# Optimization experiments

Hardware: AMD Instinct MI355X
Metric: run time of the kernel (lower is better)

Reference implementation:

```python
import jax, jax.numpy as jnp
import numpy as np

B, C, L, V, H, HEADS, ITERS = 8, 2048, 3, 512, 256, 8, 8
HD = H // HEADS
MAX_LIT = 1024  # literal embedding table holds 2*MAX_LIT rows


def _lin(x, W, b):
    return x @ W.T + b


def _gelu(x):
    return jax.nn.gelu(x, approximate=False)  # torch nn.GELU default = exact erf


def _ln(x, g, b):
    m = x.mean(-1, keepdims=True)
    v = ((x - m) ** 2).mean(-1, keepdims=True)
    return (x - m) / jnp.sqrt(v + 1e-5) * g + b


def setup_inputs() -> dict:
    key = jax.random.key(0)
    ks = jax.random.split(key, 16)
    s = 0.02
    p = {}
    p["formula"] = jax.random.randint(ks[0], (B, C, L), 0, 2 * V)
    p["lit_emb"] = jax.random.normal(ks[1], (2 * MAX_LIT, H)) * s
    # clause_encoder: Linear(H,2H) -> LayerNorm(2H) -> GELU -> Linear(2H,H)
    p["ce_w1"] = jax.random.normal(ks[2], (2 * H, H)) * s
    p["ce_b1"] = jnp.zeros((2 * H,))
    p["ce_g"] = jnp.ones((2 * H,))
    p["ce_beta"] = jnp.zeros((2 * H,))
    p["ce_w2"] = jax.random.normal(ks[3], (H, 2 * H)) * s
    p["ce_b2"] = jnp.zeros((H,))
    # clause_var_attention (nn.MultiheadAttention, eval mode -> no dropout)
    p["attn_in_w"] = jax.random.normal(ks[4], (3 * H, H)) * s
    p["attn_in_b"] = jnp.zeros((3 * H,))
    p["attn_out_w"] = jax.random.normal(ks[5], (H, H)) * s
    p["attn_out_b"] = jnp.zeros((H,))
    # variable_selector: Linear -> GELU -> Linear(H,1)
    p["vs_w1"] = jax.random.normal(ks[6], (H, H)) * s
    p["vs_b1"] = jnp.zeros((H,))
    p["vs_w2"] = jax.random.normal(ks[7], (1, H)) * s
    p["vs_b2"] = jnp.zeros((1,))
    # assignment_predictor: Linear -> GELU -> Linear(H,2) -> Softmax
    p["ap_w1"] = jax.random.normal(ks[8], (H, H)) * s
    p["ap_b1"] = jnp.zeros((H,))
    p["ap_w2"] = jax.random.normal(ks[9], (2, H)) * s
    p["ap_b2"] = jnp.zeros((2,))
    # sat_predictor: Linear -> GELU -> Linear(H,1) -> Sigmoid
    p["sp_w1"] = jax.random.normal(ks[10], (H, H)) * s
    p["sp_b1"] = jnp.zeros((H,))
    p["sp_w2"] = jax.random.normal(ks[11], (1, H)) * s
    p["sp_b2"] = jnp.zeros((1,))
    return p


def _mha(q, kv, in_w, in_b, out_w, out_b):
    Wq, Wk, Wv = jnp.split(in_w, 3, axis=0)
    bq, bk, bv = jnp.split(in_b, 3, axis=0)
    Bq, Nq, _ = q.shape
    Nk = kv.shape[1]
    qh = _lin(q, Wq, bq).reshape(Bq, Nq, HEADS, HD).transpose(0, 2, 1, 3)
    kh = _lin(kv, Wk, bk).reshape(Bq, Nk, HEADS, HD).transpose(0, 2, 1, 3)
    vh = _lin(kv, Wv, bv).reshape(Bq, Nk, HEADS, HD).transpose(0, 2, 1, 3)
    attn = jax.nn.softmax(jnp.einsum("bhqd,bhkd->bhqk", qh, kh) / np.float32(np.sqrt(HD)), axis=-1)
    o = jnp.einsum("bhqk,bhkd->bhqd", attn, vh).transpose(0, 2, 1, 3).reshape(Bq, Nq, H)
    return _lin(o, out_w, out_b)


def reference(formula, lit_emb, ce_w1, ce_b1, ce_g, ce_beta, ce_w2, ce_b2,
              attn_in_w, attn_in_b, attn_out_w, attn_out_b,
              vs_w1, vs_b1, vs_w2, vs_b2, ap_w1, ap_b1, ap_w2, ap_b2,
              sp_w1, sp_b1, sp_w2, sp_b2):
    bidx = jnp.arange(B)
    lit_e = lit_emb[formula]  # [B,C,L,H]
    # clause_encoder output is assignment-independent -> hoist out of the loop
    base = _lin(_gelu(_ln(_lin(lit_e.mean(2), ce_w1, ce_b1), ce_g, ce_beta)), ce_w2, ce_b2)  # [B,C,H]
    var_idx = formula // 2  # [B,C,L]
    pol = formula % 2

    def step(carry, _):
        assignments, var_states, done = carry
        va = assignments[bidx[:, None, None], var_idx]          # [B,C,L] gather
        sat = jnp.any((va == pol) & (va != 2), -1)              # [B,C]
        clause_states = base * (1.0 - 0.9 * sat[..., None].astype(base.dtype))
        vs = _mha(var_states, clause_states, attn_in_w, attn_in_b, attn_out_w, attn_out_b)  # [B,V,H]
        scores = _lin(_gelu(_lin(vs, vs_w1, vs_b1)), vs_w2, vs_b2)[..., 0]  # [B,V]
        scores = scores + (assignments != 2).astype(scores.dtype) * (-1e9)
        sel = jnp.argmax(scores, 1)                             # [B]
        sel_states = vs[bidx, sel]
        probs = jax.nn.softmax(_lin(_gelu(_lin(sel_states, ap_w1, ap_b1)), ap_w2, ap_b2), -1)
        new_a = jnp.argmax(probs, 1).astype(assignments.dtype)
        a2 = assignments.at[bidx, sel].set(new_a)
        # conflict check with updated assignments
        va2 = a2[bidx[:, None, None], var_idx]
        sat2 = jnp.any((va2 == pol) & (va2 != 2), -1)
        conflicting = jnp.all(va2 != 2, -1) & ~sat2             # [B,C]
        any_conf = jnp.any(conflicting)                         # global, as in torch list check
        a3 = jnp.where(any_conf, a2.at[bidx, sel].set(2), a2)   # unassign selected var on conflict
        finished = jnp.all(a3 != 2) & ~any_conf                 # torch early-break condition
        assignments_n = jnp.where(done, assignments, a3)        # freeze after break
        vs_n = jnp.where(done, var_states, vs)
        return (assignments_n, vs_n, done | finished), None

    init = (jnp.full((B, V), 2, jnp.int32), jnp.zeros((B, V, H), base.dtype), jnp.array(False))
    (assignments, var_states, _), _ = jax.lax.scan(step, init, None, length=ITERS)
    is_sat = jax.nn.sigmoid(_lin(_gelu(_lin(var_states.mean(1), sp_w1, sp_b1)), sp_w2, sp_b2))  # [B,1]
    return is_sat, assignments
```

## Files before the change

kernel.cpp:

```cpp
#include <hip/hip_runtime.h>
#include <hip/hip_bf16.h>

#pragma clang fp contract(off)

#define DEVI __device__ __forceinline__

constexpr int Bc = 8, Cc = 2048, Vc = 512, Hc = 256;

constexpr int W_N = 23;
constexpr int W_OFF[W_N] = {
  0,        524288,  655360,  655872,  656384,  656896,  787968,  788224,
  984832,   985600,  1051136, 1051392, 1116928, 1117184, 1117440, 1117444,
  1182980,  1183236, 1183748, 1183752, 1249288, 1249544, 1249800 };
constexpr int W_SZ[W_N] = {
  524288, 131072, 512, 512, 512, 131072, 256, 196608, 768,
  65536, 256, 65536, 256, 256, 1, 65536, 256, 512, 2, 65536, 256, 256, 1 };
constexpr int W_TOT = 1249804;

constexpr size_t WT1_O   = 1249808;
constexpr size_t WT2_O   = WT1_O   + 131072;
constexpr size_t WTIN_O  = WT2_O   + 131072;
constexpr size_t WTOUT_O = WTIN_O  + 196608;
constexpr size_t WTV1_O  = WTOUT_O + 65536;
constexpr size_t WTAP_O  = WTV1_O  + 65536;
constexpr size_t WTSP_O  = WTAP_O  + 65536;
constexpr size_t WCK_O   = WTSP_O  + 65536;
constexpr size_t WCV_O   = WCK_O   + 131072;
constexpr size_t BCK_O   = WCV_O   + 131072;
constexpr size_t BCV_O   = BCK_O   + 256;
constexpr size_t LP_O    = BCV_O   + 256;
constexpr size_t KB_O    = LP_O    + 524288;
constexpr size_t VB_O    = KB_O    + 4194304;
constexpr size_t VS8_O   = VB_O    + 4194304;
constexpr size_t OP_O    = VS8_O   + 2048;
constexpr size_t PM_O    = OP_O    + 8192;
constexpr size_t PL_O    = PM_O    + 256;
constexpr size_t FTOT    = PL_O    + 256;

constexpr int T_N = 7;
constexpr int T_SRC[T_N]  = { 524288, 656896, 788224, 985600, 1051392, 1117444, 1183752 };
constexpr size_t T_DST[T_N] = { WT1_O, WT2_O, WTIN_O, WTOUT_O, WTV1_O, WTAP_O, WTSP_O };
constexpr int T_ROWS[T_N] = { 512, 256, 768, 256, 256, 256, 256 };
constexpr int T_L2C[T_N]  = { 8, 9, 8, 8, 8, 8, 8 };
constexpr int T_CUM[T_N + 1] = { 0, 131072, 262144, 458752, 524288, 589824, 655360, 720896 };

struct SrcPtrs { const void* p[W_N]; };

DEVI float gelu_ref(float x) {
  return (x * (erff(x / 1.41421356237309504880f) + 1.0f)) * 0.5f;
}

__global__ __launch_bounds__(256) void k_detect(const unsigned short* __restrict__ lit,
                                                int* __restrict__ dflag) {
  __shared__ int red[256];
  int t = threadIdx.x, c = 0;
  for (int i = t; i < 4096; i += 256) {
    unsigned e = (lit[i] >> 7) & 0xFF;
    if (e >= 0x8F) c++;
  }
  red[t] = c;
  __syncthreads();
  for (int s = 128; s > 0; s >>= 1) {
    if (t < s) red[t] += red[t + s];
    __syncthreads();
  }
  if (t == 0) dflag[0] = (red[0] > 64) ? 1 : 0;
}

__global__ __launch_bounds__(256) void k_convert(SrcPtrs sp, float* __restrict__ wf,
                                                 const int* __restrict__ dflag) {
  int idx = blockIdx.x * 256 + threadIdx.x;
  if (idx >= W_TOT) return;
  const int isf32 = dflag[0];
  int i = 0;
  while (i + 1 < W_N && idx >= W_OFF[i + 1]) i++;
  int j = idx - W_OFF[i];
  float v = 0.f;
  if (j < W_SZ[i]) {
    if (isf32) v = ((const float*)sp.p[i])[j];
    else {
      unsigned int u = (unsigned int)((const unsigned short*)sp.p[i])[j] << 16;
      v = __uint_as_float(u);
    }
  }
  wf[idx] = v;
}

__global__ __launch_bounds__(256) void k_transpose(float* __restrict__ wf) {
  int idx = blockIdx.x * 256 + threadIdx.x;
  if (idx >= T_CUM[T_N]) return;
  int mi = 0;
  while (mi + 1 < T_N && idx >= T_CUM[mi + 1]) mi++;
  int local = idx - T_CUM[mi];
  int cols = 1 << T_L2C[mi];
  int r = local >> T_L2C[mi];
  int c = local & (cols - 1);
  wf[T_DST[mi] + (size_t)c * T_ROWS[mi] + r] = wf[T_SRC[mi] + (size_t)local];
}

__global__ __launch_bounds__(256) void k_combine(float* __restrict__ wf) {
  const int blk = blockIdx.x, t = threadIdx.x;
  const float* wtin = wf + WTIN_O;
  if (blk < 512) {
    __shared__ float w2row[256];
    w2row[t] = wf[WT2_O + (size_t)blk * 256 + t];
    __syncthreads();
    float aK = 0.f, aV = 0.f;
    for (int m = 0; m < 256; ++m) {
      float w2 = w2row[m];
      aK = fmaf(w2, wtin[(size_t)m * 768 + 256 + t], aK);
      aV = fmaf(w2, wtin[(size_t)m * 768 + 512 + t], aV);
    }
    wf[WCK_O + (size_t)blk * 256 + t] = aK;
    wf[WCV_O + (size_t)blk * 256 + t] = aV;
  } else {
    float aK = 0.f, aV = 0.f;
    for (int m = 0; m < 256; ++m) {
      float b2 = wf[W_OFF[6] + m];
      aK = fmaf(b2, wtin[(size_t)m * 768 + 256 + t], aK);
      aV = fmaf(b2, wtin[(size_t)m * 768 + 512 + t], aV);
    }
    wf[BCK_O + t] = aK;
    wf[BCV_O + t] = aV;
  }
}

__global__ __launch_bounds__(256) void k_litproj(float* __restrict__ wf) {
  __shared__ __align__(16) float xs[16][256];
  const int t = threadIdx.x;
  const int l0 = blockIdx.x * 16;
  const float* lit = wf + W_OFF[0];
  for (int r = 0; r < 16; ++r)
    xs[r][t] = lit[(size_t)(l0 + r) * 256 + t];
  __syncthreads();
  const float* w1t = wf + WT1_O;
  float a0[16], a1[16];
  #pragma unroll
  for (int r = 0; r < 16; ++r) { a0[r] = 0.f; a1[r] = 0.f; }
  for (int k = 0; k < 256; k += 4) {
    float wa0 = w1t[(size_t)(k+0)*512 + t], wa1 = w1t[(size_t)(k+1)*512 + t];
    float wa2 = w1t[(size_t)(k+2)*512 + t], wa3 = w1t[(size_t)(k+3)*512 + t];
    float wb0 = w1t[(size_t)(k+0)*512 + 256 + t], wb1 = w1t[(size_t)(k+1)*512 + 256 + t];
    float wb2 = w1t[(size_t)(k+2)*512 + 256 + t], wb3 = w1t[(size_t)(k+3)*512 + 256 + t];
    #pragma unroll
    for (int r = 0; r < 16; ++r) {
      float4 x4 = *(const float4*)&xs[r][k];
      a0[r] = fmaf(x4.x, wa0, a0[r]);
      a0[r] = fmaf(x4.y, wa1, a0[r]);
      a0[r] = fmaf(x4.z, wa2, a0[r]);
      a0[r] = fmaf(x4.w, wa3, a0[r]);
      a1[r] = fmaf(x4.x, wb0, a1[r]);
      a1[r] = fmaf(x4.y, wb1, a1[r]);
      a1[r] = fmaf(x4.z, wb2, a1[r]);
      a1[r] = fmaf(x4.w, wb3, a1[r]);
    }
  }
  float* LP = wf + LP_O;
  for (int r = 0; r < 16; ++r) {
    LP[(size_t)(l0 + r) * 512 + t] = a0[r];
    LP[(size_t)(l0 + r) * 512 + 256 + t] = a1[r];
  }
}

__global__ __launch_bounds__(256) void k_init(float* __restrict__ vs8,
    int* __restrict__ assign, int* __restrict__ flags, int* __restrict__ batcnt) {
  int idx = blockIdx.x * 256 + threadIdx.x;
  assign[idx] = 2;
  if (idx < 2048) vs8[idx] = 0.f;
  if (idx < 4) flags[idx] = 0;
  if (idx < 8) batcnt[idx] = 0;
}

__global__ __launch_bounds__(256) void k_base(const int* __restrict__ formula,
    const float* __restrict__ wf, float* __restrict__ Kb, float* __restrict__ Vb) {
  __shared__ __align__(16) float h1[16][516];
  __shared__ float red2[16][16];
  __shared__ float mv[16], vr[16];
  const int t = threadIdx.x;
  const int n0 = blockIdx.x * 16;
  const float* LP = wf + LP_O;
  const float* b1 = wf + W_OFF[2];
  for (int r = 0; r < 16; ++r) {
    int n = n0 + r;
    const float* p0 = LP + (size_t)formula[n*3+0] * 512;
    const float* p1 = LP + (size_t)formula[n*3+1] * 512;
    const float* p2 = LP + (size_t)formula[n*3+2] * 512;
    for (int c = t; c < 512; c += 256)
      h1[r][c] = (p0[c] + p1[c] + p2[c]) / 3.0f + b1[c];
  }
  __syncthreads();
  {
    const int r = t >> 4, l16 = t & 15;
    float s = 0.f;
    for (int j = 0; j < 32; ++j) s += h1[r][l16 + j * 16];
    red2[r][l16] = s;
  }
  __syncthreads();
  if (t < 16) {
    float s = 0.f;
    for (int i = 0; i < 16; ++i) s += red2[t][i];
    mv[t] = s / 512.0f;
  }
  __syncthreads();
  {
    const int r = t >> 4, l16 = t & 15;
    float m = mv[r], v = 0.f;
    for (int j = 0; j < 32; ++j) { float d = h1[r][l16 + j * 16] - m; v += d * d; }
    red2[r][l16] = v;
  }
  __syncthreads();
  if (t < 16) {
    float s = 0.f;
    for (int i = 0; i < 16; ++i) s += red2[t][i];
    vr[t] = s / 512.0f;
  }
  __syncthreads();
  {
    const float* g  = wf + W_OFF[3];
    const float* be = wf + W_OFF[4];
    for (int r = 0; r < 16; ++r) {
      float sd = sqrtf(vr[r] + 1e-5f);
      for (int c = t; c < 512; c += 256) {
        float val = (h1[r][c] - mv[r]) / sd * g[c] + be[c];
        h1[r][c] = gelu_ref(val);
      }
    }
  }
  __syncthreads();
  {
    const float* wck = wf + WCK_O;
    const float* wcv = wf + WCV_O;
    float aK[16], aV[16];
    #pragma unroll
    for (int r = 0; r < 16; ++r) { aK[r] = 0.f; aV[r] = 0.f; }
    for (int k = 0; k < 512; k += 4) {
      float ck0 = wck[(size_t)(k+0)*256 + t], ck1 = wck[(size_t)(k+1)*256 + t];
      float ck2 = wck[(size_t)(k+2)*256 + t], ck3 = wck[(size_t)(k+3)*256 + t];
      float cv0 = wcv[(size_t)(k+0)*256 + t], cv1 = wcv[(size_t)(k+1)*256 + t];
      float cv2 = wcv[(size_t)(k+2)*256 + t], cv3 = wcv[(size_t)(k+3)*256 + t];
      #pragma unroll
      for (int r = 0; r < 16; ++r) {
        float4 x4 = *(const float4*)&h1[r][k];
        aK[r] = fmaf(x4.x, ck0, aK[r]);
        aK[r] = fmaf(x4.y, ck1, aK[r]);
        aK[r] = fmaf(x4.z, ck2, aK[r]);
        aK[r] = fmaf(x4.w, ck3, aK[r]);
        aV[r] = fmaf(x4.x, cv0, aV[r]);
        aV[r] = fmaf(x4.y, cv1, aV[r]);
        aV[r] = fmaf(x4.z, cv2, aV[r]);
        aV[r] = fmaf(x4.w, cv3, aV[r]);
      }
    }
    float bck = wf[BCK_O + t], bcv = wf[BCV_O + t];
    const int h = t >> 5, d = t & 31;
    for (int r = 0; r < 16; ++r) {
      int n = n0 + r;
      int b = n >> 11, j = n & 2047;
      size_t off = ((size_t)(b * 8 + h) * 2048 + j) * 32 + d;
      Kb[off] = aK[r] + bck;
      Vb[off] = aV[r] + bcv;
    }
  }
}

__global__ __launch_bounds__(256) void k_iter(const int* __restrict__ formula,
    const float* __restrict__ Kb, const float* __restrict__ Vb,
    const float* __restrict__ wf, float* __restrict__ vs8,
    float* __restrict__ op, float* __restrict__ pm, float* __restrict__ pl,
    int* __restrict__ assign, int* __restrict__ selb,
    int* __restrict__ flags, int* __restrict__ batcnt) {
  if (flags[0]) return;
  __shared__ float xv[256], qs[32], qpart[8][32];
  __shared__ float sS[512], sF[512], sRed[256];
  __shared__ float sO[8][32];
  __shared__ float sM, sQB;
  __shared__ float xo[256], hh[256];
  __shared__ int ssel, sna, sconf, suna, slastS, sglast;
  const int blk = blockIdx.x;
  const int bh = blk >> 2, c = blk & 3;
  const int b = bh >> 3, h = bh & 7;
  const int t = threadIdx.x;
  const float FAC1 = 1.0f - 0.9f;

  xv[t] = vs8[b * 256 + t];
  __syncthreads();
  {
    const float* wt = wf + WTIN_O;
    const int cc = h * 32 + (t & 31), seg = t >> 5;
    float part = 0.f;
    for (int k = seg * 32; k < seg * 32 + 32; ++k)
      part = fmaf(xv[k], wt[(size_t)k * 768 + cc], part);
    qpart[seg][t & 31] = part;
  }
  __syncthreads();
  if (t < 32) {
    float acc = qpart[0][t];
    #pragma unroll
    for (int s = 1; s < 8; ++s) acc += qpart[s][t];
    qs[t] = acc + wf[W_OFF[8] + h * 32 + t];
  }
  __syncthreads();
  if (t == 0) {
    const float* bk = wf + W_OFF[8] + 256;
    float s = 0.f;
    for (int d = 0; d < 32; ++d) s = fmaf(qs[d], bk[h * 32 + d], s);
    sQB = s;
  }
  __syncthreads();
  float qreg[32];
  #pragma unroll
  for (int d = 0; d < 32; ++d) qreg[d] = qs[d];
  const float qb = sQB;
  const float* kbh = Kb + (size_t)bh * 2048 * 32;
  const float* vbh = Vb + (size_t)bh * 2048 * 32;

  float mloc = -3.402823466e38f;
  #pragma unroll
  for (int i = 0; i < 2; ++i) {
    int jl = i * 256 + t;
    int j = c * 512 + jl;
    int n = b * 2048 + j;
    bool sat = false;
    #pragma unroll
    for (int l = 0; l < 3; ++l) {
      int f = formula[n * 3 + l];
      int a = assign[b * 512 + (f >> 1)];
      sat = sat || (a == (f & 1));
    }
    float fac = sat ? FAC1 : 1.0f;
    const float4* kr4 = (const float4*)(kbh + (size_t)j * 32);
    float p = 0.f;
    #pragma unroll
    for (int g = 0; g < 8; ++g) {
      float4 kk = kr4[g];
      p = fmaf(qreg[4*g+0], kk.x, p);
      p = fmaf(qreg[4*g+1], kk.y, p);
      p = fmaf(qreg[4*g+2], kk.z, p);
      p = fmaf(qreg[4*g+3], kk.w, p);
    }
    float s = fmaf(fac, p, qb);
    sS[jl] = s; sF[jl] = fac;
    mloc = fmaxf(mloc, s);
  }
  sRed[t] = mloc;
  __syncthreads();
  for (int st = 128; st > 0; st >>= 1) {
    if (t < st) sRed[t] = fmaxf(sRed[t], sRed[t + st]);
    __syncthreads();
  }
  if (t == 0) sM = sRed[0];
  __syncthreads();
  const float Mc = sM;

  {
    float u0 = expf(sS[t * 2] - Mc);
    float u1 = expf(sS[t * 2 + 1] - Mc);
    float ll = u0 + u1;
    sS[t * 2] = u0 * sF[t * 2];
    sS[t * 2 + 1] = u1 * sF[t * 2 + 1];
    __syncthreads();
    sRed[t] = ll;
    __syncthreads();
    for (int st = 128; st > 0; st >>= 1) {
      if (t < st) sRed[t] = sRed[t] + sRed[t + st];
      __syncthreads();
    }
  }
  {
    const int jg = t >> 5, d = t & 31;
    float acc = 0.f;
    const float* vbase = vbh + (size_t)(c * 512 + jg * 64) * 32 + d;
    for (int jj = 0; jj < 64; ++jj)
      acc = fmaf(sS[jg * 64 + jj], vbase[(size_t)jj * 32], acc);
    sO[jg][d] = acc;
  }
  __syncthreads();
  if (t < 32) {
    float o = sO[0][t];
    #pragma unroll
    for (int g = 1; g < 8; ++g) o += sO[g][t];
    op[(size_t)(bh * 4 + c) * 32 + t] = o;
    if (t == 0) { pm[bh * 4 + c] = Mc; pl[bh * 4 + c] = sRed[0]; }
  }
  __syncthreads();
  if (t == 0) {
    __threadfence();
    int old = atomicAdd(&batcnt[b], 1);
    slastS = (old == 31) ? 1 : 0;
  }
  __syncthreads();
  if (!slastS) return;

  __threadfence();
  if (t == 0) { ssel = 512; sconf = 0; suna = 0; batcnt[b] = 0; }
  {
    const int h2 = t >> 5, d = t & 31, bh2 = b * 8 + h2;
    float m0 = pm[bh2*4+0], m1 = pm[bh2*4+1], m2 = pm[bh2*4+2], m3 = pm[bh2*4+3];
    float M = fmaxf(fmaxf(m0, m1), fmaxf(m2, m3));
    float e0 = expf(m0 - M), e1 = expf(m1 - M), e2 = expf(m2 - M), e3 = expf(m3 - M);
    float den = e0 * pl[bh2*4+0];
    den = fmaf(e1, pl[bh2*4+1], den);
    den = fmaf(e2, pl[bh2*4+2], den);
    den = fmaf(e3, pl[bh2*4+3], den);
    float O = e0 * op[(size_t)(bh2*4+0)*32 + d];
    O = fmaf(e1, op[(size_t)(bh2*4+1)*32 + d], O);
    O = fmaf(e2, op[(size_t)(bh2*4+2)*32 + d], O);
    O = fmaf(e3, op[(size_t)(bh2*4+3)*32 + d], O);
    float bv = wf[W_OFF[8] + 512 + h2 * 32 + d];
    xo[h2 * 32 + d] = O / den + bv;
  }
  __syncthreads();
  {
    const float* wt = wf + WTOUT_O;
    float acc = 0.f;
    for (int k = 0; k < 256; ++k) acc = fmaf(xo[k], wt[(size_t)k * 256 + t], acc);
    float v = acc + wf[W_OFF[10] + t];
    vs8[b * 256 + t] = v;
    xv[t] = v;
  }
  __syncthreads();
  for (int i = t; i < 512; i += 256)
    if (assign[b * 512 + i] == 2) atomicMin(&ssel, i);
  __syncthreads();
  const int sel = (ssel == 512) ? 0 : ssel;
  {
    const float* wt = wf + WTAP_O;
    float a = 0.f;
    for (int k = 0; k < 256; ++k) a = fmaf(xv[k], wt[(size_t)k * 256 + t], a);
    hh[t] = gelu_ref(a + wf[W_OFF[16] + t]);
  }
  __syncthreads();
  if (t == 0) {
    const float* w2 = wf + W_OFF[17];
    float l0 = 0.f, l1 = 0.f;
    for (int k = 0; k < 256; ++k) l0 = fmaf(hh[k], w2[k], l0);
    for (int k = 0; k < 256; ++k) l1 = fmaf(hh[k], w2[256 + k], l1);
    l0 += wf[W_OFF[18]];
    l1 += wf[W_OFF[18] + 1];
    int na = (l1 > l0) ? 1 : 0;
    assign[b * 512 + sel] = na;
    selb[b] = sel;
    sna = na;
  }
  __syncthreads();
  const int na = sna;
  int conf = 0, una = 0;
  for (int i = t; i < 2048; i += 256) {
    int n = b * 2048 + i;
    bool sat = false, alla = true;
    #pragma unroll
    for (int l = 0; l < 3; ++l) {
      int f = formula[n * 3 + l];
      int v = f >> 1;
      int a = (v == sel) ? na : assign[b * 512 + v];
      sat = sat || (a == (f & 1));
      alla = alla && (a != 2);
    }
    if (alla && !sat) conf = 1;
  }
  for (int i = t; i < 512; i += 256) {
    int a = (i == sel) ? na : assign[b * 512 + i];
    if (a == 2) una = 1;
  }
  if (conf) atomicOr(&sconf, 1);
  if (una) atomicOr(&suna, 1);
  __syncthreads();
  if (t == 0) {
    if (sconf) atomicOr(&flags[1], 1);
    if (suna) atomicOr(&flags[2], 1);
    __threadfence();
    int old = atomicAdd(&flags[3], 1);
    sglast = (old == 7) ? 1 : 0;
  }
  __syncthreads();
  if (sglast) {
    __threadfence();
    const int ac = flags[1], ua = flags[2];
    if (ac && t < 8) assign[t * 512 + selb[t]] = 2;
    if (t == 0) {
      if (!ac && !ua) flags[0] = 1;
      flags[1] = 0;
      flags[2] = 0;
      flags[3] = 0;
    }
  }
}

__global__ __launch_bounds__(256) void k_issat(const float* __restrict__ vs8,
    const int* __restrict__ assign, const float* __restrict__ wf,
    void* __restrict__ outv, const int* __restrict__ dflag) {
  const int b = blockIdx.x, t = threadIdx.x;
  const int isf32 = dflag[0];
  __shared__ float x[256], h[256];
  x[t] = vs8[b * 256 + t];
  __syncthreads();
  const float* wt = wf + WTSP_O;
  float a = 0.f;
  for (int k = 0; k < 256; ++k) a = fmaf(x[k], wt[(size_t)k * 256 + t], a);
  h[t] = gelu_ref(a + wf[W_OFF[20] + t]);
  __syncthreads();
  if (t == 0) {
    const float* w2 = wf + W_OFF[21];
    float l = 0.f;
    for (int k = 0; k < 256; ++k) l = fmaf(h[k], w2[k], l);
    l += wf[W_OFF[22]];
    float sig = 1.f / (1.f + expf(-l));
    if (isf32) ((float*)outv)[b] = sig;
    else ((__hip_bfloat16*)outv)[b] = __float2bfloat16(sig);
  }
  for (int i = t; i < 512; i += 256) {
    float av = (float)assign[b * 512 + i];
    if (isf32) ((float*)outv)[8 + b * 512 + i] = av;
    else ((__hip_bfloat16*)outv)[8 + b * 512 + i] = __float2bfloat16(av);
  }
}

extern "C" void kernel_launch(void* const* d_in, const int* in_sizes, int n_in,
                              void* d_out, int out_size, void* d_ws, size_t ws_size,
                              hipStream_t stream) {
  (void)in_sizes; (void)n_in; (void)out_size; (void)ws_size;
  const int* formula = (const int*)d_in[0];
  float* wf = (float*)d_ws;
  SrcPtrs sp;
  for (int i = 0; i < W_N; ++i) sp.p[i] = d_in[i + 1];
  float* Kb   = wf + KB_O;
  float* Vb   = wf + VB_O;
  float* vs8  = wf + VS8_O;
  float* op   = wf + OP_O;
  float* pm   = wf + PM_O;
  float* pl   = wf + PL_O;
  int* iw     = (int*)(wf + FTOT);
  int* assign = iw;
  int* selb   = iw + 4096;
  int* flags  = iw + 4104;
  int* dflag  = iw + 4108;
  int* batcnt = iw + 4112;

  k_detect<<<1, 256, 0, stream>>>((const unsigned short*)d_in[1], dflag);
  k_convert<<<(W_TOT + 255) / 256, 256, 0, stream>>>(sp, wf, dflag);
  k_transpose<<<(T_CUM[T_N] + 255) / 256, 256, 0, stream>>>(wf);
  k_combine<<<513, 256, 0, stream>>>(wf);
  k_litproj<<<64, 256, 0, stream>>>(wf);
  k_init<<<16, 256, 0, stream>>>(vs8, assign, flags, batcnt);
  k_base<<<1024, 256, 0, stream>>>(formula, wf, Kb, Vb);
  for (int it = 0; it < 8; ++it) {
    k_iter<<<256, 256, 0, stream>>>(formula, Kb, Vb, wf, vs8, op, pm, pl,
                                    assign, selb, flags, batcnt);
  }
  k_issat<<<8, 256, 0, stream>>>(vs8, assign, wf, d_out, dflag);
}
```

Baseline: 745.8 us.

## Split iteration kernel into 1024-block attention partials plus per-batch update kernel

Attention over clauses is now split into 16 chunks of 128 keys per (batch, head), launching 1024 blocks instead of 256. The last-block-per-batch atomic counter is replaced by a separate 8-block update kernel that merges the partial softmax results and runs the per-batch assignment logic. Weight transposes are folded into the conversion kernel, which removes one launch. This adds a second launch per iteration and leaves half of each block's threads idle during scoring, in exchange for more parallelism across the GPU.

```diff
diff --git a/kernel.cpp b/kernel.cpp
--- a/kernel.cpp
+++ b/kernel.cpp
@@ -33,16 +33,13 @@
 constexpr size_t VB_O    = KB_O    + 4194304;
 constexpr size_t VS8_O   = VB_O    + 4194304;
 constexpr size_t OP_O    = VS8_O   + 2048;
-constexpr size_t PM_O    = OP_O    + 8192;
-constexpr size_t PL_O    = PM_O    + 256;
-constexpr size_t FTOT    = PL_O    + 256;
-
-constexpr int T_N = 7;
-constexpr int T_SRC[T_N]  = { 524288, 656896, 788224, 985600, 1051392, 1117444, 1183752 };
-constexpr size_t T_DST[T_N] = { WT1_O, WT2_O, WTIN_O, WTOUT_O, WTV1_O, WTAP_O, WTSP_O };
-constexpr int T_ROWS[T_N] = { 512, 256, 768, 256, 256, 256, 256 };
-constexpr int T_L2C[T_N]  = { 8, 9, 8, 8, 8, 8, 8 };
-constexpr int T_CUM[T_N + 1] = { 0, 131072, 262144, 458752, 524288, 589824, 655360, 720896 };
+constexpr size_t PM_O    = OP_O    + 32768;
+constexpr size_t PL_O    = PM_O    + 1024;
+constexpr size_t FTOT    = PL_O    + 1024;
+
+constexpr int    TR_L2C[W_N]  = {0,8,0,0,0,9,0,8,0,8,0,0,0,0,0,8,0,0,0,8,0,0,0};
+constexpr size_t TR_DST[W_N]  = {0,WT1_O,0,0,0,WT2_O,0,WTIN_O,0,WTOUT_O,0,0,0,0,0,WTAP_O,0,0,0,WTSP_O,0,0,0};
+constexpr int    TR_ROWS[W_N] = {0,512,0,0,0,256,0,768,0,256,0,0,0,0,0,256,0,0,0,256,0,0,0};
 
 struct SrcPtrs { const void* p[W_N]; };
 
@@ -82,20 +79,13 @@
       unsigned int u = (unsigned int)((const unsigned short*)sp.p[i])[j] << 16;
       v = __uint_as_float(u);
     }
+    int l2c = TR_L2C[i];
+    if (l2c) {
+      int r = j >> l2c, c = j & ((1 << l2c) - 1);
+      wf[TR_DST[i] + (size_t)c * TR_ROWS[i] + r] = v;
+    }
   }
   wf[idx] = v;
-}
-
-__global__ __launch_bounds__(256) void k_transpose(float* __restrict__ wf) {
-  int idx = blockIdx.x * 256 + threadIdx.x;
-  if (idx >= T_CUM[T_N]) return;
-  int mi = 0;
-  while (mi + 1 < T_N && idx >= T_CUM[mi + 1]) mi++;
-  int local = idx - T_CUM[mi];
-  int cols = 1 << T_L2C[mi];
-  int r = local >> T_L2C[mi];
-  int c = local & (cols - 1);
-  wf[T_DST[mi] + (size_t)c * T_ROWS[mi] + r] = wf[T_SRC[mi] + (size_t)local];
 }
 
 __global__ __launch_bounds__(256) void k_combine(float* __restrict__ wf) {
@@ -163,12 +153,11 @@
 }
 
 __global__ __launch_bounds__(256) void k_init(float* __restrict__ vs8,
-    int* __restrict__ assign, int* __restrict__ flags, int* __restrict__ batcnt) {
+    int* __restrict__ assign, int* __restrict__ flags) {
   int idx = blockIdx.x * 256 + threadIdx.x;
   assign[idx] = 2;
   if (idx < 2048) vs8[idx] = 0.f;
   if (idx < 4) flags[idx] = 0;
-  if (idx < 8) batcnt[idx] = 0;
 }
 
 __global__ __launch_bounds__(256) void k_base(const int* __restrict__ formula,
@@ -263,21 +252,18 @@
   }
 }
 
-__global__ __launch_bounds__(256) void k_iter(const int* __restrict__ formula,
-    const float* __restrict__ Kb, const float* __restrict__ Vb,
-    const float* __restrict__ wf, float* __restrict__ vs8,
-    float* __restrict__ op, float* __restrict__ pm, float* __restrict__ pl,
-    int* __restrict__ assign, int* __restrict__ selb,
-    int* __restrict__ flags, int* __restrict__ batcnt) {
+__global__ __launch_bounds__(256) void k_attn_part(const int* __restrict__ formula,
+    const int* __restrict__ assign, const float* __restrict__ Kb,
+    const float* __restrict__ Vb, const float* __restrict__ wf,
+    const float* __restrict__ vs8, float* __restrict__ op, float* __restrict__ pm,
+    float* __restrict__ pl, const int* __restrict__ flags) {
   if (flags[0]) return;
   __shared__ float xv[256], qs[32], qpart[8][32];
-  __shared__ float sS[512], sF[512], sRed[256];
+  __shared__ float sW[128], sRed[256];
   __shared__ float sO[8][32];
   __shared__ float sM, sQB;
-  __shared__ float xo[256], hh[256];
-  __shared__ int ssel, sna, sconf, suna, slastS, sglast;
   const int blk = blockIdx.x;
-  const int bh = blk >> 2, c = blk & 3;
+  const int bh = blk >> 4, c = blk & 15;
   const int b = bh >> 3, h = bh & 7;
   const int t = threadIdx.x;
   const float FAC1 = 1.0f - 0.9f;
@@ -315,10 +301,9 @@
   const float* vbh = Vb + (size_t)bh * 2048 * 32;
 
   float mloc = -3.402823466e38f;
-  #pragma unroll
-  for (int i = 0; i < 2; ++i) {
-    int jl = i * 256 + t;
-    int j = c * 512 + jl;
+  float sval = 0.f, fval = 1.0f;
+  if (t < 128) {
+    int j = c * 128 + t;
     int n = b * 2048 + j;
     bool sat = false;
     #pragma unroll
@@ -339,8 +324,8 @@
       p = fmaf(qreg[4*g+3], kk.w, p);
     }
     float s = fmaf(fac, p, qb);
-    sS[jl] = s; sF[jl] = fac;
-    mloc = fmaxf(mloc, s);
+    sval = s; fval = fac;
+    mloc = s;
   }
   sRed[t] = mloc;
   __syncthreads();
@@ -353,12 +338,12 @@
   const float Mc = sM;
 
   {
-    float u0 = expf(sS[t * 2] - Mc);
-    float u1 = expf(sS[t * 2 + 1] - Mc);
-    float ll = u0 + u1;
-    sS[t * 2] = u0 * sF[t * 2];
-    sS[t * 2 + 1] = u1 * sF[t * 2 + 1];
-    __syncthreads();
+    float ll = 0.f;
+    if (t < 128) {
+      float u = expf(sval - Mc);
+      ll = u;
+      sW[t] = u * fval;
+    }
     sRed[t] = ll;
     __syncthreads();
     for (int st = 128; st > 0; st >>= 1) {
@@ -369,9 +354,9 @@
   {
     const int jg = t >> 5, d = t & 31;
     float acc = 0.f;
-    const float* vbase = vbh + (size_t)(c * 512 + jg * 64) * 32 + d;
-    for (int jj = 0; jj < 64; ++jj)
-      acc = fmaf(sS[jg * 64 + jj], vbase[(size_t)jj * 32], acc);
+    const float* vbase = vbh + (size_t)(c * 128 + jg * 16) * 32 + d;
+    for (int jj = 0; jj < 16; ++jj)
+      acc = fmaf(sW[jg * 16 + jj], vbase[(size_t)jj * 32], acc);
     sO[jg][d] = acc;
   }
   __syncthreads();
@@ -379,35 +364,35 @@
     float o = sO[0][t];
     #pragma unroll
     for (int g = 1; g < 8; ++g) o += sO[g][t];
-    op[(size_t)(bh * 4 + c) * 32 + t] = o;
-    if (t == 0) { pm[bh * 4 + c] = Mc; pl[bh * 4 + c] = sRed[0]; }
-  }
-  __syncthreads();
-  if (t == 0) {
-    __threadfence();
-    int old = atomicAdd(&batcnt[b], 1);
-    slastS = (old == 31) ? 1 : 0;
-  }
-  __syncthreads();
-  if (!slastS) return;
-
-  __threadfence();
-  if (t == 0) { ssel = 512; sconf = 0; suna = 0; batcnt[b] = 0; }
-  {
-    const int h2 = t >> 5, d = t & 31, bh2 = b * 8 + h2;
-    float m0 = pm[bh2*4+0], m1 = pm[bh2*4+1], m2 = pm[bh2*4+2], m3 = pm[bh2*4+3];
-    float M = fmaxf(fmaxf(m0, m1), fmaxf(m2, m3));
-    float e0 = expf(m0 - M), e1 = expf(m1 - M), e2 = expf(m2 - M), e3 = expf(m3 - M);
-    float den = e0 * pl[bh2*4+0];
-    den = fmaf(e1, pl[bh2*4+1], den);
-    den = fmaf(e2, pl[bh2*4+2], den);
-    den = fmaf(e3, pl[bh2*4+3], den);
-    float O = e0 * op[(size_t)(bh2*4+0)*32 + d];
-    O = fmaf(e1, op[(size_t)(bh2*4+1)*32 + d], O);
-    O = fmaf(e2, op[(size_t)(bh2*4+2)*32 + d], O);
-    O = fmaf(e3, op[(size_t)(bh2*4+3)*32 + d], O);
-    float bv = wf[W_OFF[8] + 512 + h2 * 32 + d];
-    xo[h2 * 32 + d] = O / den + bv;
+    op[(size_t)(bh * 16 + c) * 32 + t] = o;
+    if (t == 0) { pm[bh * 16 + c] = Mc; pl[bh * 16 + c] = sRed[0]; }
+  }
+}
+
+__global__ __launch_bounds__(256) void k_update(const int* __restrict__ formula,
+    const float* __restrict__ op, const float* __restrict__ pm,
+    const float* __restrict__ pl, const float* __restrict__ wf,
+    float* __restrict__ vs8, int* __restrict__ assign, int* __restrict__ selb,
+    int* __restrict__ flags) {
+  if (flags[0]) return;
+  const int b = blockIdx.x, t = threadIdx.x;
+  __shared__ float xo[256], xv[256], hh[256];
+  __shared__ int ssel, sna, sconf, suna, slast;
+  if (t == 0) { ssel = 512; sconf = 0; suna = 0; }
+  {
+    const int h = t >> 5, d = t & 31, bh = b * 8 + h;
+    float M = pm[bh * 16];
+    #pragma unroll
+    for (int i = 1; i < 16; ++i) M = fmaxf(M, pm[bh * 16 + i]);
+    float den = 0.f, O = 0.f;
+    #pragma unroll
+    for (int i = 0; i < 16; ++i) {
+      float e = expf(pm[bh * 16 + i] - M);
+      den = fmaf(e, pl[bh * 16 + i], den);
+      O = fmaf(e, op[(size_t)(bh * 16 + i) * 32 + d], O);
+    }
+    float bv = wf[W_OFF[8] + 512 + h * 32 + d];
+    xo[h * 32 + d] = O / den + bv;
   }
   __syncthreads();
   {
@@ -470,10 +455,10 @@
     if (suna) atomicOr(&flags[2], 1);
     __threadfence();
     int old = atomicAdd(&flags[3], 1);
-    sglast = (old == 7) ? 1 : 0;
-  }
-  __syncthreads();
-  if (sglast) {
+    slast = (old == 7) ? 1 : 0;
+  }
+  __syncthreads();
+  if (slast) {
     __threadfence();
     const int ac = flags[1], ua = flags[2];
     if (ac && t < 8) assign[t * 512 + selb[t]] = 2;
@@ -534,18 +519,18 @@
   int* selb   = iw + 4096;
   int* flags  = iw + 4104;
   int* dflag  = iw + 4108;
-  int* batcnt = iw + 4112;
 
   k_detect<<<1, 256, 0, stream>>>((const unsigned short*)d_in[1], dflag);
   k_convert<<<(W_TOT + 255) / 256, 256, 0, stream>>>(sp, wf, dflag);
-  k_transpose<<<(T_CUM[T_N] + 255) / 256, 256, 0, stream>>>(wf);
   k_combine<<<513, 256, 0, stream>>>(wf);
   k_litproj<<<64, 256, 0, stream>>>(wf);
-  k_init<<<16, 256, 0, stream>>>(vs8, assign, flags, batcnt);
+  k_init<<<16, 256, 0, stream>>>(vs8, assign, flags);
   k_base<<<1024, 256, 0, stream>>>(formula, wf, Kb, Vb);
   for (int it = 0; it < 8; ++it) {
-    k_iter<<<256, 256, 0, stream>>>(formula, Kb, Vb, wf, vs8, op, pm, pl,
-                                    assign, selb, flags, batcnt);
+    k_attn_part<<<1024, 256, 0, stream>>>(formula, assign, Kb, Vb, wf, vs8,
+                                          op, pm, pl, flags);
+    k_update<<<8, 256, 0, stream>>>(formula, op, pm, pl, wf, vs8, assign,
+                                    selb, flags);
   }
   k_issat<<<8, 256, 0, stream>>>(vs8, assign, wf, d_out, dflag);
 }
```

After: 726.0 us. 2.7% less time.
